# Performance work log

Measured on AMD Instinct MI355X. Metric: run time of the kernel, lower is better.

The kernel has to match this reference:

```python
import jax, jax.numpy as jnp
import numpy as np

EMBD, DIM, HEADS, FF = 768, 64, 12, 4
B, T = 4, 2048
LN_EPS = 1e-5


def setup_inputs() -> dict:
    key = jax.random.key(0)
    ks = jax.random.split(key, 8)
    dh = DIM * HEADS
    inp = {
        "x": jax.random.normal(ks[0], (B, T, EMBD), jnp.float32),
        "ln_g": jnp.ones((EMBD,), jnp.float32),
        "ln_b": jnp.zeros((EMBD,), jnp.float32),
        # weights stored [in, out] for x @ W
        "w_qkv": jax.random.normal(ks[1], (EMBD, 3 * dh), jnp.float32) * (EMBD ** -0.5),
        "w_attn_out": jax.random.normal(ks[2], (dh, EMBD), jnp.float32) * (dh ** -0.5),
        "w_in": jax.random.normal(ks[3], (EMBD, EMBD * FF), jnp.float32) * (EMBD ** -0.5),
        "b_in": jnp.zeros((EMBD * FF,), jnp.float32),
        "w_out": jax.random.normal(ks[4], (EMBD * FF, EMBD), jnp.float32) * ((EMBD * FF) ** -0.5),
        "b_out": jnp.zeros((EMBD,), jnp.float32),
    }
    return inp


def _layernorm(x, g, b):
    mu = jnp.mean(x, axis=-1, keepdims=True)
    var = jnp.mean(jnp.square(x - mu), axis=-1, keepdims=True)
    return (x - mu) * jax.lax.rsqrt(var + LN_EPS) * g + b


def reference(x, ln_g, ln_b, w_qkv, w_attn_out, w_in, b_in, w_out, b_out):
    norm = _layernorm(x, ln_g, ln_b)  # [B,T,E]
    # qkv packed as (k, d, h) along last dim per einops 'b t (k d h)'
    qkv = norm @ w_qkv  # [B,T,3*D*H]
    qkv = qkv.reshape(B, T, 3, DIM, HEADS)
    qkv = jnp.transpose(qkv, (2, 0, 4, 1, 3))  # [3,B,H,T,D]
    q, k, v = qkv[0], qkv[1], qkv[2]
    scale = DIM ** -0.5
    dots = jnp.einsum('bhid,bhjd->bhij', q, k) * scale  # [B,H,T,T]
    attn = jax.nn.softmax(dots, axis=-1)
    out = jnp.einsum('bhij,bhjd->bhid', attn, v)  # [B,H,T,D]
    out = jnp.transpose(out, (0, 2, 1, 3)).reshape(B, T, HEADS * DIM)  # 'b h t d -> b t (h d)'
    x = x + out @ w_attn_out
    # MLP branch consumes `norm` (faithful to the original module)
    h = jax.nn.gelu(norm @ w_in + b_in, approximate=False)
    x = x + h @ w_out + b_out
    return x
```

## Files before the change

### kernel.cpp

```cpp
#include <hip/hip_runtime.h>
#include <math.h>

typedef __bf16 bf16;
typedef __bf16 bf16x8 __attribute__((ext_vector_type(8)));
typedef __bf16 bf16x4 __attribute__((ext_vector_type(4)));
typedef float  f32x4  __attribute__((ext_vector_type(4)));
typedef unsigned int u32;

#define MFMA16(a, b, c) __builtin_amdgcn_mfma_f32_16x16x32_bf16((a), (b), (c), 0, 0, 0)

__device__ __forceinline__ void async_copy16(const bf16* g, bf16* l) {
  __builtin_amdgcn_global_load_lds((const __attribute__((address_space(1))) void*)g,
                                   (__attribute__((address_space(3))) void*)l, 16, 0, 0);
}

__device__ __forceinline__ float fast_exp2(float x) {
#if __has_builtin(__builtin_amdgcn_exp2f)
  return __builtin_amdgcn_exp2f(x);
#else
  float r; asm("v_exp_f32 %0, %1" : "=v"(r) : "v"(x)); return r;
#endif
}

__global__ __launch_bounds__(256) void ln_kernel(const float* __restrict__ x,
    const float* __restrict__ g, const float* __restrict__ b, bf16* __restrict__ nrm) {
  const int tok = blockIdx.x, t = threadIdx.x;
  const float* xr = x + (size_t)tok * 768;
  float v0 = xr[t], v1 = xr[t + 256], v2 = xr[t + 512];
  float s = v0 + v1 + v2, ss = v0 * v0 + v1 * v1 + v2 * v2;
  for (int off = 32; off; off >>= 1) {
    s += __shfl_down(s, off, 64); ss += __shfl_down(ss, off, 64);
  }
  __shared__ float red[8];
  if ((t & 63) == 0) { red[(t >> 6) * 2] = s; red[(t >> 6) * 2 + 1] = ss; }
  __syncthreads();
  s = red[0] + red[2] + red[4] + red[6];
  ss = red[1] + red[3] + red[5] + red[7];
  float mu = s * (1.f / 768.f);
  float rstd = rsqrtf(ss * (1.f / 768.f) - mu * mu + 1e-5f);
  bf16* o = nrm + (size_t)tok * 768;
  o[t]       = (bf16)((v0 - mu) * rstd * g[t]       + b[t]);
  o[t + 256] = (bf16)((v1 - mu) * rstd * g[t + 256] + b[t + 256]);
  o[t + 512] = (bf16)((v2 - mu) * rstd * g[t + 512] + b[t + 512]);
}

template <int PERM>
__global__ __launch_bounds__(256) void castT_kernel(const float* __restrict__ in,
    bf16* __restrict__ out, int K, int N) {
  __shared__ float tile[64][65];
  const int t = threadIdx.x;
  const int r = t >> 4, c4 = (t & 15) * 4;
  const int k0 = blockIdx.y * 64, n0 = blockIdx.x * 64;
  for (int it = 0; it < 4; ++it) {
    int row = r + it * 16;
    const float4 v = *(const float4*)(in + (size_t)(k0 + row) * N + n0 + c4);
    tile[row][c4] = v.x; tile[row][c4 + 1] = v.y;
    tile[row][c4 + 2] = v.z; tile[row][c4 + 3] = v.w;
  }
  __syncthreads();
  for (int it = 0; it < 4; ++it) {
    int row = r + it * 16;
    int n = n0 + row;
    if (PERM) {
      int which = n / 768, rem = n - which * 768;
      int d = rem / 12, h = rem - d * 12;
      n = which * 768 + h * 64 + d;
    }
    bf16x4 v;
    for (int j = 0; j < 4; ++j) v[j] = (bf16)tile[c4 + j][row];
    *(bf16x4*)(out + (size_t)n * K + k0 + c4) = v;
  }
}

template <int MT, int RES, int BIAS, int GELU, int OUTF32, int SPLIT>
__global__ __launch_bounds__(256) void gemm_bt(
    const bf16* __restrict__ A, const bf16* __restrict__ Bt, int ldb,
    void* __restrict__ Cv, const float* __restrict__ bias, const float* __restrict__ res,
    bf16* __restrict__ qo, bf16* __restrict__ ko, bf16* __restrict__ vo,
    int M, int N, int K) {
  constexpr int NJ = (MT == 128) ? 4 : 2;
  constexpr int AH = MT * 32;
  __shared__ bf16 As[2 * AH];
  __shared__ bf16 Bs[2 * 4096];
  const int t = threadIdx.x;
  const int l = t & 63, w = t >> 6;
  const int lr = l >> 4, lc = l & 15;
  const int wm = (MT == 128) ? (w >> 1) : 0;
  const int wn = (MT == 128) ? (w & 1) : w;
  const int m0 = blockIdx.y * MT, n0 = blockIdx.x * 128;

  const int srow = t >> 2;
  const int scol = (t & 3) * 8;
  const bf16* ga0 = A + (size_t)(m0 + srow) * K + scol;
  const bf16* ga1 = A + (size_t)(m0 + 64 + srow) * K + scol;
  const bf16* gb0 = Bt + (size_t)(n0 + srow) * ldb + scol;
  const bf16* gb1 = Bt + (size_t)(n0 + 64 + srow) * ldb + scol;

  f32x4 acc[4][NJ];
  for (int i = 0; i < 4; ++i)
    for (int j = 0; j < NJ; ++j) acc[i][j] = (f32x4){0.f, 0.f, 0.f, 0.f};

  for (int k0 = 0; k0 < K; k0 += 64) {
    async_copy16(ga0 + k0,      &As[w * 512]);
    async_copy16(ga0 + k0 + 32, &As[AH + w * 512]);
    if (MT == 128) {
      async_copy16(ga1 + k0,      &As[2048 + w * 512]);
      async_copy16(ga1 + k0 + 32, &As[AH + 2048 + w * 512]);
    }
    async_copy16(gb0 + k0,      &Bs[w * 512]);
    async_copy16(gb0 + k0 + 32, &Bs[4096 + w * 512]);
    async_copy16(gb1 + k0,      &Bs[2048 + w * 512]);
    async_copy16(gb1 + k0 + 32, &Bs[4096 + 2048 + w * 512]);
    __syncthreads();
    for (int h = 0; h < 2; ++h) {
      bf16x8 af[4], bfr[NJ];
      for (int i = 0; i < 4; ++i)
        af[i] = *(const bf16x8*)&As[h * AH + (wm * 64 + i * 16 + lc) * 32 + 8 * lr];
      for (int j = 0; j < NJ; ++j)
        bfr[j] = *(const bf16x8*)&Bs[h * 4096 + (wn * 16 * NJ + j * 16 + lc) * 32 + 8 * lr];
      for (int i = 0; i < 4; ++i)
        for (int j = 0; j < NJ; ++j)
          acc[i][j] = MFMA16(af[i], bfr[j], acc[i][j]);
    }
    __syncthreads();
  }

  const size_t Ns = (size_t)N;
  for (int i = 0; i < 4; ++i) {
    int rowb = m0 + wm * 64 + i * 16 + lr * 4;
    for (int j = 0; j < NJ; ++j) {
      int col = n0 + wn * 16 * NJ + j * 16 + lc;
      float bv = BIAS ? bias[col] : 0.f;
      for (int r = 0; r < 4; ++r) {
        int row = rowb + r;
        float vv = acc[i][j][r];
        if (BIAS) vv += bv;
        if (GELU) vv = 0.5f * vv * (1.f + erff(vv * 0.70710678118654752f));
        if (RES)  vv += res[(size_t)row * Ns + col];
        if (SPLIT) {
          int which = col / 768;
          int rem = col - which * 768;
          int h = rem >> 6, d = rem & 63;
          int bb = row >> 11, tt = row & 2047;
          if (which == 2) {
            int T = tt >> 6, k2 = tt & 63;
            int sv = (k2 & 32) | ((k2 & 12) << 1) | ((k2 & 16) >> 2) | (k2 & 3);
            int pos = ((((sv >> 3) ^ (d & 7)) << 3) | (sv & 7));
            vo[(size_t)(bb * 12 + h) * 131072 + (size_t)T * 4096 + d * 64 + pos] = (bf16)vv;
          } else {
            if (which == 0) vv *= 0.18033688011112042f;
            bf16* dst = which == 0 ? qo : ko;
            dst[((size_t)((bb * 12 + h) * 2048 + tt)) * 64 + d] = (bf16)vv;
          }
        } else if (OUTF32) {
          ((float*)Cv)[(size_t)row * Ns + col] = vv;
        } else {
          ((bf16*)Cv)[(size_t)row * Ns + col] = (bf16)vv;
        }
      }
    }
  }
}

__global__ __launch_bounds__(128) void attn_kernel(const bf16* __restrict__ q,
    const bf16* __restrict__ k, const bf16* __restrict__ v, bf16* __restrict__ out) {
  __shared__ bf16 Ks0[4096], Ks1[4096], Vs0[4096], Vs1[4096];
  const int t = threadIdx.x;
  const int l = t & 63, w = t >> 6;
  const int g = l >> 4, c = l & 15;
  const int id = blockIdx.y * 16 + blockIdx.x;
  const int swz = (id & 7) * 96 + (id >> 3);
  const int bh = swz >> 4;
  const int q0 = (swz & 15) * 128;
  const size_t base = (size_t)bh * (2048 * 64);
  const int qr = q0 + w * 64;
  bf16x8 aq[4][2];
  for (int rt = 0; rt < 4; ++rt) {
    aq[rt][0] = *(const bf16x8*)(q + base + (size_t)(qr + rt * 16 + c) * 64 + 8 * g);
    aq[rt][1] = *(const bf16x8*)(q + base + (size_t)(qr + rt * 16 + c) * 64 + 32 + 8 * g);
  }
  f32x4 O[4][4], O5[4];
  for (int rt = 0; rt < 4; ++rt) {
    for (int j = 0; j < 4; ++j) O[rt][j] = (f32x4){0.f, 0.f, 0.f, 0.f};
    O5[rt] = (f32x4){0.f, 0.f, 0.f, 0.f};
  }
  bf16x8 ones;
  for (int i = 0; i < 8; ++i) ones[i] = (bf16)1.0f;

  const bf16* kt = k + base + (size_t)(8 * w + (l >> 3)) * 64 + ((l & 7) ^ (l >> 3)) * 8;
  const bf16* vt = v + base + w * 512 + l * 8;
  const int pk0 = (g ^ (c & 7)) * 8;
  const int pk1 = ((4 + g) ^ (c & 7)) * 8;

  auto stage = [&](const bf16* kp, const bf16* vp, bf16* KsD, bf16* VsD) {
    #pragma unroll
    for (int r = 0; r < 4; ++r) {
      async_copy16(kp + r * 1024, KsD + w * 512 + r * 1024);
      async_copy16(vp + r * 1024, VsD + w * 512 + r * 1024);
    }
  };

  auto compute = [&](const bf16* KsP, const bf16* VsP) {
    bf16x8 ap[4][2];
    #pragma unroll
    for (int m = 0; m < 4; ++m) {
      bf16x8 b0 = *(const bf16x8*)&KsP[(16 * m + c) * 64 + pk0];
      bf16x8 b1 = *(const bf16x8*)&KsP[(16 * m + c) * 64 + pk1];
      f32x4 Sm[4];
      #pragma unroll
      for (int rt = 0; rt < 4; ++rt) {
        f32x4 z = (f32x4){0.f, 0.f, 0.f, 0.f};
        z = MFMA16(b0, aq[rt][0], z);
        Sm[rt] = MFMA16(b1, aq[rt][1], z);
      }
      #pragma unroll
      for (int rt = 0; rt < 4; ++rt)
        #pragma unroll
        for (int r = 0; r < 4; ++r)
          ap[rt][m >> 1][(m & 1) * 4 + r] = (bf16)fast_exp2(Sm[rt][r]);
    }
    #pragma unroll
    for (int j = 0; j < 4; ++j) {
      bf16x8 bv0 = *(const bf16x8*)&VsP[(16 * j + c) * 64 + pk0];
      bf16x8 bv1 = *(const bf16x8*)&VsP[(16 * j + c) * 64 + pk1];
      #pragma unroll
      for (int rt = 0; rt < 4; ++rt) {
        O[rt][j] = MFMA16(ap[rt][0], bv0, O[rt][j]);
        O[rt][j] = MFMA16(ap[rt][1], bv1, O[rt][j]);
      }
    }
    #pragma unroll
    for (int rt = 0; rt < 4; ++rt) {
      O5[rt] = MFMA16(ap[rt][0], ones, O5[rt]);
      O5[rt] = MFMA16(ap[rt][1], ones, O5[rt]);
    }
  };

  stage(kt, vt, Ks0, Vs0);
  kt += 4096; vt += 4096;
  bf16 *ka = Ks0, *kb = Ks1, *va = Vs0, *vb = Vs1;
  for (int i = 0; i < 32; ++i) {
    __builtin_amdgcn_s_barrier();
    if (i + 1 < 32) {
      stage(kt, vt, kb, vb);
      kt += 4096; vt += 4096;
      asm volatile("s_waitcnt vmcnt(8)" ::: "memory");
    } else {
      asm volatile("s_waitcnt vmcnt(0)" ::: "memory");
    }
    __builtin_amdgcn_sched_barrier(0);
    __builtin_amdgcn_s_barrier();
    compute(ka, va);
    bf16* tmp;
    tmp = ka; ka = kb; kb = tmp;
    tmp = va; va = vb; vb = tmp;
  }

  const int b = bh / 12, h = bh % 12;
  for (int rt = 0; rt < 4; ++rt)
    for (int r = 0; r < 4; ++r) {
      float inv = 1.0f / O5[rt][r];
      int tok = q0 + w * 64 + rt * 16 + g * 4 + r;
      for (int j = 0; j < 4; ++j) {
        int col = h * 64 + j * 16 + c;
        out[(size_t)(b * 2048 + tok) * 768 + col] = (bf16)(O[rt][j][r] * inv);
      }
    }
}

extern "C" void kernel_launch(void* const* d_in, const int* in_sizes, int n_in,
                              void* d_out, int out_size, void* d_ws, size_t ws_size,
                              hipStream_t stream) {
  static const long expected[9] = {6291456, 768, 768, 1769472, 589824, 2359296,
                                   3072, 2359296, 768};
  long f = 1; bool found = false;
  for (long ff = 1; ff <= 4 && !found; ff *= 2)
    for (int i = 0; i < n_in; ++i)
      if ((long)in_sizes[i] == 6291456L * ff) { f = ff; found = true; break; }
  int idx[9]; bool used[32] = {false};
  for (int s = 0; s < 9; ++s) {
    idx[s] = -1;
    if (found)
      for (int i = 0; i < n_in; ++i)
        if (!used[i] && (long)in_sizes[i] == expected[s] * f) { idx[s] = i; used[i] = true; break; }
    if (idx[s] < 0) idx[s] = s;
  }
  const float* x    = (const float*)d_in[idx[0]];
  const float* ln_g = (const float*)d_in[idx[1]];
  const float* ln_b = (const float*)d_in[idx[2]];
  const float* wqkv = (const float*)d_in[idx[3]];
  const float* wao  = (const float*)d_in[idx[4]];
  const float* wi   = (const float*)d_in[idx[5]];
  const float* bi   = (const float*)d_in[idx[6]];
  const float* wo   = (const float*)d_in[idx[7]];
  const float* bo   = (const float*)d_in[idx[8]];

  char* ws = (char*)d_ws;
  bf16*  norm = (bf16*)(ws);
  bf16*  wtq  = (bf16*)(ws + 12582912);
  bf16*  at   = (bf16*)(ws + 12582912);
  bf16*  qb   = (bf16*)(ws + 25165824);
  bf16*  wta  = (bf16*)(ws + 25165824);
  bf16*  kb   = (bf16*)d_out;
  bf16*  vb   = (bf16*)((char*)d_out + 12582912);
  float* x1   = (float*)d_out;

  const bool big = ws_size >= 72351744ULL;
  bf16* hbuf = (bf16*)(ws + 12582912);
  bf16* wti  = big ? (bf16*)(ws + 62914560) : (bf16*)(ws + 26345472);
  bf16* wto  = big ? (bf16*)(ws + 67633152) : (bf16*)(ws + 31064064);

  ln_kernel<<<8192, 256, 0, stream>>>(x, ln_g, ln_b, norm);
  castT_kernel<1><<<dim3(36, 12), 256, 0, stream>>>(wqkv, wtq, 768, 2304);
  gemm_bt<128,0,0,0,0,1><<<dim3(18, 64), 256, 0, stream>>>(
      norm, wtq, 768, nullptr, nullptr, nullptr, qb, kb, vb, 8192, 2304, 768);
  attn_kernel<<<dim3(16, 48), 128, 0, stream>>>(qb, kb, vb, at);
  castT_kernel<0><<<dim3(12, 12), 256, 0, stream>>>(wao, wta, 768, 768);
  castT_kernel<0><<<dim3(48, 12), 256, 0, stream>>>(wi,  wti, 768, 3072);
  castT_kernel<0><<<dim3(12, 48), 256, 0, stream>>>(wo,  wto, 3072, 768);
  gemm_bt<64,1,0,0,1,0><<<dim3(6, 128), 256, 0, stream>>>(
      at, wta, 768, x1, nullptr, x, nullptr, nullptr, nullptr, 8192, 768, 768);
  if (big) {
    gemm_bt<64,0,1,1,0,0><<<dim3(24, 128), 256, 0, stream>>>(
        norm, wti, 768, hbuf, bi, nullptr, nullptr, nullptr, nullptr, 8192, 3072, 768);
    gemm_bt<64,1,1,0,1,0><<<dim3(6, 128), 256, 0, stream>>>(
        hbuf, wto, 3072, x1, bo, x1, nullptr, nullptr, nullptr, 8192, 768, 3072);
  } else {
    for (int p = 0; p < 4; ++p) {
      gemm_bt<64,0,1,1,0,0><<<dim3(6, 128), 256, 0, stream>>>(
          norm, wti + (size_t)p * 768 * 768, 768, hbuf, bi + p * 768, nullptr,
          nullptr, nullptr, nullptr, 8192, 768, 768);
      if (p < 3)
        gemm_bt<64,1,0,0,1,0><<<dim3(6, 128), 256, 0, stream>>>(
            hbuf, wto + (size_t)p * 768, 3072, x1, nullptr, x1,
            nullptr, nullptr, nullptr, 8192, 768, 768);
      else
        gemm_bt<64,1,1,0,1,0><<<dim3(6, 128), 256, 0, stream>>>(
            hbuf, wto + (size_t)p * 768, 3072, x1, bo, x1,
            nullptr, nullptr, nullptr, 8192, 768, 768);
    }
  }
}
```

Before: 397.6 us.

## Split attention KV range across block pairs and use polynomial erf in GELU

Attention blocks now cover 256 queries with 4 waves and handle half of the key/value sequence each. The two blocks of a pair combine partial outputs and denominators through workspace buffers and an atomic flag handshake, with the second arriver spin-waiting before it normalizes. This is meant to raise per-block query reuse of K/V tiles while keeping the grid size the same. The exact erff in the GELU epilogue is replaced with an Abramowitz-Stegun polynomial built on fast rcp/exp2, which lowers accuracy slightly. The spin-wait assumes both blocks of a pair are resident at once, which risks deadlock or stalls if they are not co-scheduled.

```diff
diff --git a/kernel.cpp b/kernel.cpp
--- a/kernel.cpp
+++ b/kernel.cpp
@@ -20,6 +20,24 @@
 #else
   float r; asm("v_exp_f32 %0, %1" : "=v"(r) : "v"(x)); return r;
 #endif
+}
+
+__device__ __forceinline__ float fast_rcp(float x) {
+#if __has_builtin(__builtin_amdgcn_rcpf)
+  return __builtin_amdgcn_rcpf(x);
+#else
+  float r; asm("v_rcp_f32 %0, %1" : "=v"(r) : "v"(x)); return r;
+#endif
+}
+
+__device__ __forceinline__ float fast_erff(float x) {
+  float ax = fabsf(x);
+  float t = fast_rcp(1.0f + 0.3275911f * ax);
+  float p = t * (0.254829592f + t * (-0.284496736f + t * (1.421413741f +
+            t * (-1.453152027f + t * 1.061405429f))));
+  float e = fast_exp2(-ax * ax * 1.4426950408889634f);
+  float r = 1.0f - p * e;
+  return x < 0.0f ? -r : r;
 }
 
 __global__ __launch_bounds__(256) void ln_kernel(const float* __restrict__ x,
@@ -43,6 +61,8 @@
   o[t + 256] = (bf16)((v1 - mu) * rstd * g[t + 256] + b[t + 256]);
   o[t + 512] = (bf16)((v2 - mu) * rstd * g[t + 512] + b[t + 512]);
 }
+
+__global__ void flags_clear(int* __restrict__ f) { f[threadIdx.x] = 0; }
 
 template <int PERM>
 __global__ __launch_bounds__(256) void castT_kernel(const float* __restrict__ in,
@@ -135,7 +155,7 @@
         int row = rowb + r;
         float vv = acc[i][j][r];
         if (BIAS) vv += bv;
-        if (GELU) vv = 0.5f * vv * (1.f + erff(vv * 0.70710678118654752f));
+        if (GELU) vv = 0.5f * vv * (1.f + fast_erff(vv * 0.70710678118654752f));
         if (RES)  vv += res[(size_t)row * Ns + col];
         if (SPLIT) {
           int which = col / 768;
@@ -162,16 +182,20 @@
   }
 }
 
-__global__ __launch_bounds__(128) void attn_kernel(const bf16* __restrict__ q,
-    const bf16* __restrict__ k, const bf16* __restrict__ v, bf16* __restrict__ out) {
+__global__ __launch_bounds__(256) void attn_kernel(const bf16* __restrict__ q,
+    const bf16* __restrict__ k, const bf16* __restrict__ v, bf16* __restrict__ out,
+    float* __restrict__ pO, float* __restrict__ pD, int* __restrict__ flags) {
   __shared__ bf16 Ks0[4096], Ks1[4096], Vs0[4096], Vs1[4096];
+  __shared__ int sflag;
   const int t = threadIdx.x;
   const int l = t & 63, w = t >> 6;
   const int g = l >> 4, c = l & 15;
   const int id = blockIdx.y * 16 + blockIdx.x;
   const int swz = (id & 7) * 96 + (id >> 3);
   const int bh = swz >> 4;
-  const int q0 = (swz & 15) * 128;
+  const int rem = swz & 15;
+  const int qb = rem >> 1, hf = rem & 1;
+  const int q0 = qb * 256;
   const size_t base = (size_t)bh * (2048 * 64);
   const int qr = q0 + w * 64;
   bf16x8 aq[4][2];
@@ -187,17 +211,17 @@
   bf16x8 ones;
   for (int i = 0; i < 8; ++i) ones[i] = (bf16)1.0f;
 
-  const bf16* kt = k + base + (size_t)(8 * w + (l >> 3)) * 64 + ((l & 7) ^ (l >> 3)) * 8;
-  const bf16* vt = v + base + w * 512 + l * 8;
+  const bf16* kt = k + base + (size_t)hf * 65536
+                   + (size_t)(8 * w + (l >> 3)) * 64 + ((l & 7) ^ (l >> 3)) * 8;
+  const bf16* vt = v + base + (size_t)hf * 65536 + w * 512 + l * 8;
   const int pk0 = (g ^ (c & 7)) * 8;
   const int pk1 = ((4 + g) ^ (c & 7)) * 8;
 
   auto stage = [&](const bf16* kp, const bf16* vp, bf16* KsD, bf16* VsD) {
-    #pragma unroll
-    for (int r = 0; r < 4; ++r) {
-      async_copy16(kp + r * 1024, KsD + w * 512 + r * 1024);
-      async_copy16(vp + r * 1024, VsD + w * 512 + r * 1024);
-    }
+    async_copy16(kp,        KsD + w * 512);
+    async_copy16(kp + 2048, KsD + 2048 + w * 512);
+    async_copy16(vp,        VsD + w * 512);
+    async_copy16(vp + 2048, VsD + 2048 + w * 512);
   };
 
   auto compute = [&](const bf16* KsP, const bf16* VsP) {
@@ -239,12 +263,12 @@
   stage(kt, vt, Ks0, Vs0);
   kt += 4096; vt += 4096;
   bf16 *ka = Ks0, *kb = Ks1, *va = Vs0, *vb = Vs1;
-  for (int i = 0; i < 32; ++i) {
+  for (int i = 0; i < 16; ++i) {
     __builtin_amdgcn_s_barrier();
-    if (i + 1 < 32) {
+    if (i + 1 < 16) {
       stage(kt, vt, kb, vb);
       kt += 4096; vt += 4096;
-      asm volatile("s_waitcnt vmcnt(8)" ::: "memory");
+      asm volatile("s_waitcnt vmcnt(4)" ::: "memory");
     } else {
       asm volatile("s_waitcnt vmcnt(0)" ::: "memory");
     }
@@ -256,14 +280,40 @@
     tmp = va; va = vb; vb = tmp;
   }
 
+  const int pair = bh * 8 + qb;
+  float* po = pO + (size_t)pair * 256 * 64;
+  float* pd = pD + (size_t)pair * 256;
+  if (t == 0) sflag = atomicAdd(&flags[pair], 1);
+  __syncthreads();
+  if (sflag == 0) {
+    for (int rt = 0; rt < 4; ++rt)
+      for (int r = 0; r < 4; ++r) {
+        int tok = w * 64 + rt * 16 + g * 4 + r;
+        for (int j = 0; j < 4; ++j)
+          po[(size_t)tok * 64 + j * 16 + c] = O[rt][j][r];
+        if (c == 0) pd[tok] = O5[rt][r];
+      }
+    __syncthreads();
+    if (t == 0) { __threadfence(); atomicAdd(&flags[pair], 1); }
+    return;
+  }
+  if (t == 0) {
+    while (__hip_atomic_load(&flags[pair], __ATOMIC_ACQUIRE,
+                             __HIP_MEMORY_SCOPE_AGENT) < 3)
+      __builtin_amdgcn_s_sleep(2);
+  }
+  __syncthreads();
+  __threadfence();
   const int b = bh / 12, h = bh % 12;
   for (int rt = 0; rt < 4; ++rt)
     for (int r = 0; r < 4; ++r) {
-      float inv = 1.0f / O5[rt][r];
-      int tok = q0 + w * 64 + rt * 16 + g * 4 + r;
+      int tok = w * 64 + rt * 16 + g * 4 + r;
+      float lt = O5[rt][r] + pd[tok];
+      float inv = fast_rcp(lt);
+      int gtok = q0 + tok;
       for (int j = 0; j < 4; ++j) {
-        int col = h * 64 + j * 16 + c;
-        out[(size_t)(b * 2048 + tok) * 768 + col] = (bf16)(O[rt][j][r] * inv);
+        float os = O[rt][j][r] + po[(size_t)tok * 64 + j * 16 + c];
+        out[(size_t)(b * 2048 + gtok) * 768 + h * 64 + j * 16 + c] = (bf16)(os * inv);
       }
     }
 }
@@ -305,16 +355,21 @@
   bf16*  vb   = (bf16*)((char*)d_out + 12582912);
   float* x1   = (float*)d_out;
 
+  float* pO    = (float*)(ws + 37748736);
+  float* pD    = (float*)(ws + 62914560);
+  int*   flags = (int*)(ws + 63307776);
+
   const bool big = ws_size >= 72351744ULL;
   bf16* hbuf = (bf16*)(ws + 12582912);
   bf16* wti  = big ? (bf16*)(ws + 62914560) : (bf16*)(ws + 26345472);
   bf16* wto  = big ? (bf16*)(ws + 67633152) : (bf16*)(ws + 31064064);
 
   ln_kernel<<<8192, 256, 0, stream>>>(x, ln_g, ln_b, norm);
+  flags_clear<<<1, 384, 0, stream>>>(flags);
   castT_kernel<1><<<dim3(36, 12), 256, 0, stream>>>(wqkv, wtq, 768, 2304);
   gemm_bt<128,0,0,0,0,1><<<dim3(18, 64), 256, 0, stream>>>(
       norm, wtq, 768, nullptr, nullptr, nullptr, qb, kb, vb, 8192, 2304, 768);
-  attn_kernel<<<dim3(16, 48), 128, 0, stream>>>(qb, kb, vb, at);
+  attn_kernel<<<dim3(16, 48), 256, 0, stream>>>(qb, kb, vb, at, pO, pD, flags);
   castT_kernel<0><<<dim3(12, 12), 256, 0, stream>>>(wao, wta, 768, 768);
   castT_kernel<0><<<dim3(48, 12), 256, 0, stream>>>(wi,  wti, 768, 3072);
   castT_kernel<0><<<dim3(12, 48), 256, 0, stream>>>(wo,  wto, 3072, 768);
```

Result: slower. 473.5 us (+19.1%).
